# Optimization experiments

Measured on AMD Instinct MI355X. Metric: run time of the kernel, lower is better.

Reference implementation:

```python
import jax, jax.numpy as jnp
import numpy as np

B, T, D, H = 2, 2048, 1024, 16
DK = D // H  # 64, head dim (even, required by RoPE pairing)


def setup_inputs() -> dict:
    key = jax.random.key(0)
    ks = jax.random.split(key, 9)
    sc = 1.0 / np.sqrt(D)
    x = jax.random.normal(ks[0], (B, T, D), jnp.float32)
    wq = jax.random.normal(ks[1], (D, D), jnp.float32) * sc
    bq = jax.random.normal(ks[2], (D,), jnp.float32) * 0.01
    wk = jax.random.normal(ks[3], (D, D), jnp.float32) * sc
    bk = jax.random.normal(ks[4], (D,), jnp.float32) * 0.01
    wv = jax.random.normal(ks[5], (D, D), jnp.float32) * sc
    bv = jax.random.normal(ks[6], (D,), jnp.float32) * 0.01
    wo = jax.random.normal(ks[7], (D, D), jnp.float32) * sc
    bo = jax.random.normal(ks[8], (D,), jnp.float32) * 0.01
    # causal mask, True = masked (matches masked_fill semantics); dim==3 -> broadcast over heads
    attn_mask = jnp.triu(jnp.ones((T, T), dtype=bool), 1)[None]  # [1,T,T]
    return dict(x=x, wq=wq, bq=bq, wk=wk, bk=bk, wv=wv, bv=bv, wo=wo, bo=bo,
                attn_mask=attn_mask)


def _rope(xh, sin, cos):
    # xh: [B,H,T,DK]; sin/cos: [T,DK/2]
    x1 = xh[..., 0::2]
    x2 = xh[..., 1::2]
    return jnp.stack([x1 * cos - x2 * sin, x1 * sin + x2 * cos], axis=-1).reshape(xh.shape)


def reference(x, wq, bq, wk, bk, wv, bv, wo, bo, attn_mask):
    q = (x @ wq.T + bq).reshape(B, T, H, DK).transpose(0, 2, 1, 3)  # [B,H,T,DK]
    k = (x @ wk.T + bk).reshape(B, T, H, DK).transpose(0, 2, 1, 3)
    v = (x @ wv.T + bv).reshape(B, T, H, DK).transpose(0, 2, 1, 3)
    # RoPE (seq_offset = 0)
    theta = 10000.0 ** (jnp.arange(0, DK, 2, dtype=jnp.float32) / DK)  # [DK/2]
    pos = jnp.arange(T, dtype=jnp.float32)[:, None]                    # [T,1]
    ang = pos / theta                                                  # [T,DK/2]
    sin, cos = jnp.sin(ang), jnp.cos(ang)
    q = _rope(q, sin, cos)
    k = _rope(k, sin, cos)
    # fp32 stable attention (inputs already fp32)
    scores = jnp.einsum('bhtd,bhsd->bhts', q, k) / np.sqrt(DK)
    scores = jnp.where(attn_mask[:, None], -1e9, scores)  # mask broadcast over heads
    attn = jax.nn.softmax(scores, axis=-1)
    ctx = jnp.einsum('bhts,bhsd->bhtd', attn, v)
    ctx = ctx.transpose(0, 2, 1, 3).reshape(B, T, D)
    return ctx @ wo.T + bo
```

## Files before the change

kernel.cpp:

```cpp
#include <hip/hip_runtime.h>
#include <stdint.h>
#include <stddef.h>

#define T_ 2048
#define D_ 1024
#define H_ 16

typedef __attribute__((ext_vector_type(8))) short short8;
typedef __attribute__((ext_vector_type(4))) float f32x4;
typedef __attribute__((ext_vector_type(4))) short s16x4;

__device__ __forceinline__ unsigned short f2bf(float f){
  union { float f; unsigned u; } c; c.f = f;
  unsigned u = c.u;
  return (unsigned short)((u + 0x7fffu + ((u >> 16) & 1u)) >> 16);
}

__device__ __forceinline__ unsigned pk_bf16(float lo, float hi){
  unsigned r;
  asm("v_cvt_pk_bf16_f32 %0, %1, %2" : "=v"(r) : "v"(lo), "v"(hi));
  return r;
}

__device__ __forceinline__ float fexp2(float x){
#if __has_builtin(__builtin_amdgcn_exp2f)
  return __builtin_amdgcn_exp2f(x);
#else
  return exp2f(x);
#endif
}

__device__ __forceinline__ f32x4 mfma16(short8 a, short8 b, f32x4 c){
  return __builtin_amdgcn_mfma_f32_16x16x32_bf16(a, b, c, 0, 0, 0);
}

__device__ __forceinline__ void gload16(const void* g, void* l){
  __builtin_amdgcn_global_load_lds(
      (const __attribute__((address_space(1))) unsigned*)g,
      (__attribute__((address_space(3))) unsigned*)l, 16, 0, 0);
}

__global__ __launch_bounds__(256) void k_prep(const float* __restrict__ x,
    const float* __restrict__ wq, const float* __restrict__ wk,
    const float* __restrict__ wv, const float* __restrict__ wo,
    unsigned short* __restrict__ xb, unsigned short* __restrict__ wqkv,
    unsigned short* __restrict__ wob)
{
  const long long NX = 4194304LL, NW = 1048576LL;
  long long base = ((long long)blockIdx.x * 256 + threadIdx.x) * 4;
  const float* s; unsigned short* d;
  if (base < NX){ s = x + base; d = xb + base; }
  else if (base < NX + 3*NW){
    long long j = base - NX;
    if (j < NW) s = wq + j;
    else if (j < 2*NW) s = wk + (j - NW);
    else s = wv + (j - 2*NW);
    d = wqkv + j;
  } else if (base < NX + 4*NW){
    long long j = base - NX - 3*NW;
    s = wo + j; d = wob + j;
  } else return;
  float4 v = *(const float4*)s;
  d[0] = f2bf(v.x); d[1] = f2bf(v.y); d[2] = f2bf(v.z); d[3] = f2bf(v.w);
}

__global__ __launch_bounds__(256) void k_rope(float* __restrict__ tab){
  int i = blockIdx.x * 256 + threadIdx.x;
  if (i >= T_ * 32) return;
  int t = i >> 5, p = i & 31;
  float ang = (float)t * powf(10000.0f, -(float)p * (1.0f / 32.0f));
  tab[i] = sinf(ang);
  tab[T_ * 32 + i] = cosf(ang);
}

__device__ __forceinline__ void gemm_core(const unsigned short* __restrict__ A,
    const unsigned short* __restrict__ Bm, int m0, int n0,
    unsigned short* lA, unsigned short* lB, f32x4 (&acc)[4][4])
{
  const int tid = threadIdx.x, lane = tid & 63, wave = tid >> 6;
  const int wr = wave >> 1, wc = wave & 1;
  for (int mi = 0; mi < 4; ++mi)
    for (int ni = 0; ni < 4; ++ni)
      acc[mi][ni] = (f32x4){0.f, 0.f, 0.f, 0.f};
  for (int k0 = 0; k0 < 1024; k0 += 64){
    __syncthreads();
#pragma unroll
    for (int p = 0; p < 4; ++p){
      int c = p * 256 + tid, r = c >> 3, s = c & 7;
      int gs = (s ^ (r & 7)) << 3;
      gload16(A + (size_t)(m0 + r) * 1024 + k0 + gs, lA + c * 8);
      gload16(Bm + (size_t)(n0 + r) * 1024 + k0 + gs, lB + c * 8);
    }
    __syncthreads();
#pragma unroll
    for (int kk = 0; kk < 2; ++kk){
      int kslot = kk * 4 + (lane >> 4);
      short8 af[4], bf[4];
#pragma unroll
      for (int mi = 0; mi < 4; ++mi){
        int row = wr * 64 + mi * 16 + (lane & 15);
        af[mi] = *(const short8*)(lA + row * 64 + ((kslot ^ (row & 7)) << 3));
      }
#pragma unroll
      for (int ni = 0; ni < 4; ++ni){
        int row = wc * 64 + ni * 16 + (lane & 15);
        bf[ni] = *(const short8*)(lB + row * 64 + ((kslot ^ (row & 7)) << 3));
      }
#pragma unroll
      for (int mi = 0; mi < 4; ++mi)
#pragma unroll
        for (int ni = 0; ni < 4; ++ni)
          acc[mi][ni] = mfma16(af[mi], bf[ni], acc[mi][ni]);
    }
  }
}

__global__ __launch_bounds__(256) void k_qkv(const unsigned short* __restrict__ xb,
    const unsigned short* __restrict__ wqkv,
    const float* __restrict__ bq, const float* __restrict__ bk, const float* __restrict__ bv,
    const float* __restrict__ tab,
    unsigned short* __restrict__ Qw, unsigned short* __restrict__ Kw,
    unsigned short* __restrict__ Vw)
{
  __shared__ alignas(16) unsigned short lA[128 * 64];
  __shared__ alignas(16) unsigned short lB[128 * 64];
  int m0 = blockIdx.y * 128, n0 = blockIdx.x * 128;
  f32x4 acc[4][4];
  gemm_core(xb, wqkv, m0, n0, lA, lB, acc);
  int lane = threadIdx.x & 63, wave = threadIdx.x >> 6;
  int wr = wave >> 1, wc = wave & 1;
  int mat = n0 >> 10;
  const float* bias = (mat == 0) ? bq : (mat == 1 ? bk : bv);
  const float* st = tab; const float* ct = tab + T_ * 32;
  if (mat < 2){
    unsigned short* Out = (mat == 0) ? Qw : Kw;
    float qs = (mat == 0) ? 0.18033688011116f : 1.0f;
    for (int mi = 0; mi < 4; ++mi){
      for (int ni = 0; ni < 4; ++ni){
        int col = n0 + wc * 64 + ni * 16 + (lane & 15);
        int nn = col & 1023, h = nn >> 6, dd = nn & 63;
        float bsv = bias[nn];
        f32x4 v4 = acc[mi][ni];
#pragma unroll
        for (int r = 0; r < 4; ++r){
          int m = m0 + wr * 64 + mi * 16 + ((lane >> 4) << 2) + r;
          int bb = m >> 11, t = m & 2047;
          float v = v4[r] + bsv;
          float u = __shfl_xor(v, 1);
          int p = dd >> 1;
          float sv = st[t * 32 + p], cv = ct[t * 32 + p];
          float res = (dd & 1) ? (u * sv + v * cv) : (v * cv - u * sv);
          Out[((size_t)(bb * H_ + h) * T_ + t) * 64 + dd] = f2bf(res * qs);
        }
      }
    }
  } else {
    for (int mi = 0; mi < 4; ++mi){
      for (int ni = 0; ni < 4; ++ni){
        int col = n0 + wc * 64 + ni * 16 + (lane & 15);
        int nn = col & 1023, h = nn >> 6, dd = nn & 63;
        float bsv = bias[nn];
        int mb = m0 + wr * 64 + mi * 16 + ((lane >> 4) << 2);
        int bb = mb >> 11, t = mb & 2047;
        f32x4 v4 = acc[mi][ni];
        s16x4 o;
#pragma unroll
        for (int r = 0; r < 4; ++r) o[r] = (short)f2bf(v4[r] + bsv);
        *(s16x4*)(Vw + ((size_t)((bb * H_ + h) * 64 + dd)) * T_ + t) = o;
      }
    }
  }
}

__global__ __launch_bounds__(256) void k_attn(const unsigned short* __restrict__ Qw,
    const unsigned short* __restrict__ Kw, const unsigned short* __restrict__ Vt_g,
    unsigned short* __restrict__ ctxb)
{
  __shared__ alignas(16) unsigned short Kl[64 * 64];
  __shared__ alignas(16) unsigned short Vl[64 * 64];
  int qt = (int)gridDim.y - 1 - (int)blockIdx.y;
  int bh = blockIdx.x;
  int tid = threadIdx.x, lane = tid & 63, wave = tid >> 6;
  const unsigned short* Qb = Qw + (size_t)bh * T_ * 64;
  const unsigned short* Kb = Kw + (size_t)bh * T_ * 64;
  const unsigned short* Vb = Vt_g + (size_t)bh * 64 * T_;
  int q0 = qt * 128 + wave * 32;

  short8 qf[2][2];
#pragma unroll
  for (int mi = 0; mi < 2; ++mi){
    const unsigned short* qp = Qb + (size_t)(q0 + mi * 16 + (lane & 15)) * 64 + ((lane >> 4) << 3);
    qf[mi][0] = *(const short8*)qp;
    qf[mi][1] = *(const short8*)(qp + 32);
  }
  float mr[2] = {-1e30f, -1e30f}, lr[2] = {0.f, 0.f};
  f32x4 acc_o[2][4];
#pragma unroll
  for (int mi = 0; mi < 2; ++mi)
#pragma unroll
    for (int df = 0; df < 4; ++df) acc_o[mi][df] = (f32x4){0.f, 0.f, 0.f, 0.f};

  const int src0 = ((lane >> 4) & 1) * 32 + (lane & 15);
  const int src1 = src0 + 16;
  const bool hiHalf = lane >= 32;

  int ntiles = 2 * qt + 2;
  for (int jt = 0; jt < ntiles; ++jt){
    int j0 = jt * 64;
    __syncthreads();
#pragma unroll
    for (int p = 0; p < 2; ++p){
      int c = p * 256 + tid, r = c >> 3, s = c & 7;
      int gs = (s ^ (r & 7)) << 3;
      gload16(Kb + (size_t)(j0 + r) * 64 + gs, Kl + c * 8);
      gload16(Vb + (size_t)r * T_ + j0 + gs, Vl + c * 8);
    }
    __syncthreads();
    if (j0 > q0 + 31) continue;
    bool need_mask = (j0 + 63 > q0);

    f32x4 accs[2][4];
#pragma unroll
    for (int mi = 0; mi < 2; ++mi)
#pragma unroll
      for (int jf = 0; jf < 4; ++jf) accs[mi][jf] = (f32x4){0.f, 0.f, 0.f, 0.f};
#pragma unroll
    for (int kk = 0; kk < 2; ++kk){
      int kslot = kk * 4 + (lane >> 4);
      short8 kf[4];
#pragma unroll
      for (int jf = 0; jf < 4; ++jf){
        int row = jf * 16 + (lane & 15);
        kf[jf] = *(const short8*)(Kl + row * 64 + ((kslot ^ (row & 7)) << 3));
      }
#pragma unroll
      for (int mi = 0; mi < 2; ++mi)
#pragma unroll
        for (int jf = 0; jf < 4; ++jf)
          accs[mi][jf] = mfma16(kf[jf], qf[mi][kk], accs[mi][jf]);
    }

    unsigned w0[2][4], w1[2][4];
#pragma unroll
    for (int mi = 0; mi < 2; ++mi){
      int qa = q0 + mi * 16 + (lane & 15);
      float s[4][4];
      float mx = -1e30f;
#pragma unroll
      for (int jf = 0; jf < 4; ++jf)
#pragma unroll
        for (int r = 0; r < 4; ++r){
          float sv = accs[mi][jf][r];
          if (need_mask){
            int ja = j0 + jf * 16 + ((lane >> 4) << 2) + r;
            if (ja > qa) sv = -1e30f;
          }
          s[jf][r] = sv;
          mx = fmaxf(mx, sv);
        }
      mx = fmaxf(mx, __shfl_xor(mx, 16));
      mx = fmaxf(mx, __shfl_xor(mx, 32));
      float mn = fmaxf(mr[mi], mx);
      float sc = fexp2(mr[mi] - mn);
      mr[mi] = mn;
      float rs = 0.f;
#pragma unroll
      for (int jf = 0; jf < 4; ++jf)
#pragma unroll
        for (int r = 0; r < 4; ++r){
          float pe = fexp2(s[jf][r] - mn);
          s[jf][r] = pe;
          rs += pe;
        }
      rs += __shfl_xor(rs, 16);
      rs += __shfl_xor(rs, 32);
      lr[mi] = lr[mi] * sc + rs;
#pragma unroll
      for (int df = 0; df < 4; ++df){
        f32x4 a = acc_o[mi][df];
        a[0] *= sc; a[1] *= sc; a[2] *= sc; a[3] *= sc;
        acc_o[mi][df] = a;
      }
#pragma unroll
      for (int jf = 0; jf < 4; ++jf){
        w0[mi][jf] = pk_bf16(s[jf][0], s[jf][1]);
        w1[mi][jf] = pk_bf16(s[jf][2], s[jf][3]);
      }
    }

#pragma unroll
    for (int kk = 0; kk < 2; ++kk){
      int jslot = kk * 4 + (lane >> 4);
      short8 vf[4];
#pragma unroll
      for (int df = 0; df < 4; ++df){
        int row = df * 16 + (lane & 15);
        vf[df] = *(const short8*)(Vl + row * 64 + ((jslot ^ (row & 7)) << 3));
      }
#pragma unroll
      for (int mi = 0; mi < 2; ++mi){
        unsigned lo0 = (unsigned)__shfl((int)w0[mi][2*kk],   src0);
        unsigned hi0 = (unsigned)__shfl((int)w0[mi][2*kk+1], src0);
        unsigned lo1 = (unsigned)__shfl((int)w1[mi][2*kk],   src0);
        unsigned hi1 = (unsigned)__shfl((int)w1[mi][2*kk+1], src0);
        unsigned lo2 = (unsigned)__shfl((int)w0[mi][2*kk],   src1);
        unsigned hi2 = (unsigned)__shfl((int)w0[mi][2*kk+1], src1);
        unsigned lo3 = (unsigned)__shfl((int)w1[mi][2*kk],   src1);
        unsigned hi3 = (unsigned)__shfl((int)w1[mi][2*kk+1], src1);
        union { unsigned u[4]; short8 v; } pb;
        pb.u[0] = hiHalf ? hi0 : lo0;
        pb.u[1] = hiHalf ? hi1 : lo1;
        pb.u[2] = hiHalf ? hi2 : lo2;
        pb.u[3] = hiHalf ? hi3 : lo3;
#pragma unroll
        for (int df = 0; df < 4; ++df)
          acc_o[mi][df] = mfma16(vf[df], pb.v, acc_o[mi][df]);
      }
    }
  }

  int bb = bh >> 4, h = bh & 15;
#pragma unroll
  for (int mi = 0; mi < 2; ++mi){
    float inv = 1.0f / lr[mi];
    int t = q0 + mi * 16 + (lane & 15);
#pragma unroll
    for (int df = 0; df < 4; ++df){
      int d0 = df * 16 + ((lane >> 4) << 2);
      f32x4 a = acc_o[mi][df];
      s16x4 o;
#pragma unroll
      for (int r = 0; r < 4; ++r) o[r] = (short)f2bf(a[r] * inv);
      *(s16x4*)(ctxb + ((size_t)(bb * T_ + t)) * 1024 + h * 64 + d0) = o;
    }
  }
}

__global__ __launch_bounds__(256) void k_oproj(const unsigned short* __restrict__ ctxb,
    const unsigned short* __restrict__ wob, const float* __restrict__ bo,
    float* __restrict__ out)
{
  __shared__ alignas(16) unsigned short lA[128 * 64];
  __shared__ alignas(16) unsigned short lB[128 * 64];
  int m0 = blockIdx.y * 128, n0 = blockIdx.x * 128;
  f32x4 acc[4][4];
  gemm_core(ctxb, wob, m0, n0, lA, lB, acc);
  int lane = threadIdx.x & 63, wave = threadIdx.x >> 6;
  int wr = wave >> 1, wc = wave & 1;
  for (int mi = 0; mi < 4; ++mi)
    for (int ni = 0; ni < 4; ++ni){
      int col = n0 + wc * 64 + ni * 16 + (lane & 15);
      float bsv = bo[col];
      f32x4 v4 = acc[mi][ni];
#pragma unroll
      for (int r = 0; r < 4; ++r){
        int m = m0 + wr * 64 + mi * 16 + ((lane >> 4) << 2) + r;
        out[(size_t)m * 1024 + col] = v4[r] + bsv;
      }
    }
}

extern "C" void kernel_launch(void* const* d_in, const int* in_sizes, int n_in,
                              void* d_out, int out_size, void* d_ws, size_t ws_size,
                              hipStream_t stream)
{
  const float* x  = (const float*)d_in[0];
  const float* wq = (const float*)d_in[1];
  const float* bq = (const float*)d_in[2];
  const float* wk = (const float*)d_in[3];
  const float* bk = (const float*)d_in[4];
  const float* wv = (const float*)d_in[5];
  const float* bv = (const float*)d_in[6];
  const float* wo = (const float*)d_in[7];
  const float* bo = (const float*)d_in[8];
  char* w = (char*)d_ws;
  unsigned short* xb   = (unsigned short*)(w);
  unsigned short* wqkv = (unsigned short*)(w + (8 << 20));
  unsigned short* wob  = (unsigned short*)(w + (14 << 20));
  unsigned short* Qw   = (unsigned short*)(w + (16 << 20));
  unsigned short* Kw   = (unsigned short*)(w + (24 << 20));
  unsigned short* Vw   = (unsigned short*)(w + (32 << 20));
  unsigned short* ctxb = (unsigned short*)(w + (40 << 20));
  float* tab           = (float*)(w + (48 << 20));

  k_prep<<<8192, 256, 0, stream>>>(x, wq, wk, wv, wo, xb, wqkv, wob);
  k_rope<<<256, 256, 0, stream>>>(tab);
  k_qkv<<<dim3(24, 32), 256, 0, stream>>>(xb, wqkv, bq, bk, bv, tab, Qw, Kw, Vw);
  k_attn<<<dim3(32, 16), 256, 0, stream>>>(Qw, Kw, Vw, ctxb);
  k_oproj<<<dim3(8, 32), 256, 0, stream>>>(ctxb, wob, bo, (float*)d_out);
}
```

Measured before the change: 148.4 us.

## Double-buffer attention K/V tiles, lazy softmax rescale, fuse rope into prep

The attention kernel now double-buffers K/V tiles in shared memory, issuing the next tile's async load before computing the current one, so only one barrier is needed per iteration. It hoists the V fragment reads, raises wave priority around MFMA blocks, and skips the online-softmax rescale unless the running max grows by more than a threshold. The block index is remapped to a 1D swizzled grid to change how work is spread across compute units. The RoPE table generation is folded into the prep kernel, removing one launch. Shared memory use doubles and the lazy rescale lets exponentials exceed 1 by a bounded factor, a small precision risk.

```diff
diff --git a/kernel.cpp b/kernel.cpp
--- a/kernel.cpp
+++ b/kernel.cpp
@@ -44,8 +44,15 @@
     const float* __restrict__ wq, const float* __restrict__ wk,
     const float* __restrict__ wv, const float* __restrict__ wo,
     unsigned short* __restrict__ xb, unsigned short* __restrict__ wqkv,
-    unsigned short* __restrict__ wob)
-{
+    unsigned short* __restrict__ wob, float* __restrict__ tab)
+{
+  if (blockIdx.x < 256){
+    int i = blockIdx.x * 256 + threadIdx.x;
+    int t = i >> 5, p = i & 31;
+    float ang = (float)t * powf(10000.0f, -(float)p * (1.0f / 32.0f));
+    tab[i] = sinf(ang);
+    tab[T_ * 32 + i] = cosf(ang);
+  }
   const long long NX = 4194304LL, NW = 1048576LL;
   long long base = ((long long)blockIdx.x * 256 + threadIdx.x) * 4;
   const float* s; unsigned short* d;
@@ -62,15 +69,6 @@
   } else return;
   float4 v = *(const float4*)s;
   d[0] = f2bf(v.x); d[1] = f2bf(v.y); d[2] = f2bf(v.z); d[3] = f2bf(v.w);
-}
-
-__global__ __launch_bounds__(256) void k_rope(float* __restrict__ tab){
-  int i = blockIdx.x * 256 + threadIdx.x;
-  if (i >= T_ * 32) return;
-  int t = i >> 5, p = i & 31;
-  float ang = (float)t * powf(10000.0f, -(float)p * (1.0f / 32.0f));
-  tab[i] = sinf(ang);
-  tab[T_ * 32 + i] = cosf(ang);
 }
 
 __device__ __forceinline__ void gemm_core(const unsigned short* __restrict__ A,
@@ -176,10 +174,12 @@
     const unsigned short* __restrict__ Kw, const unsigned short* __restrict__ Vt_g,
     unsigned short* __restrict__ ctxb)
 {
-  __shared__ alignas(16) unsigned short Kl[64 * 64];
-  __shared__ alignas(16) unsigned short Vl[64 * 64];
-  int qt = (int)gridDim.y - 1 - (int)blockIdx.y;
-  int bh = blockIdx.x;
+  __shared__ alignas(16) unsigned short Kl[2][64 * 64];
+  __shared__ alignas(16) unsigned short Vl[2][64 * 64];
+  int bid = blockIdx.x;
+  int swz = (bid & 7) * 64 + (bid >> 3);
+  int bh = swz >> 4;
+  int qt = 15 - (swz & 15);
   int tid = threadIdx.x, lane = tid & 63, wave = tid >> 6;
   const unsigned short* Qb = Qw + (size_t)bh * T_ * 64;
   const unsigned short* Kb = Kw + (size_t)bh * T_ * 64;
@@ -203,120 +203,143 @@
   const int src0 = ((lane >> 4) & 1) * 32 + (lane & 15);
   const int src1 = src0 + 16;
   const bool hiHalf = lane >= 32;
-
   int ntiles = 2 * qt + 2;
-  for (int jt = 0; jt < ntiles; ++jt){
-    int j0 = jt * 64;
-    __syncthreads();
+
+  auto STAGE = [&](int jt){
+    int buf = jt & 1, j0 = jt * 64;
+    unsigned short* Kd = (unsigned short*)Kl[buf];
+    unsigned short* Vd = (unsigned short*)Vl[buf];
 #pragma unroll
     for (int p = 0; p < 2; ++p){
       int c = p * 256 + tid, r = c >> 3, s = c & 7;
       int gs = (s ^ (r & 7)) << 3;
-      gload16(Kb + (size_t)(j0 + r) * 64 + gs, Kl + c * 8);
-      gload16(Vb + (size_t)r * T_ + j0 + gs, Vl + c * 8);
+      gload16(Kb + (size_t)(j0 + r) * 64 + gs, Kd + c * 8);
+      gload16(Vb + (size_t)r * T_ + j0 + gs, Vd + c * 8);
+    }
+  };
+
+  STAGE(0);
+  __syncthreads();
+  for (int jt = 0; jt < ntiles; ++jt){
+    if (jt + 1 < ntiles) STAGE(jt + 1);
+    int j0 = jt * 64;
+    if (j0 <= q0 + 31){
+      const unsigned short* Kc = Kl[jt & 1];
+      const unsigned short* Vc = Vl[jt & 1];
+      bool need_mask = (j0 + 63 > q0);
+
+      f32x4 accs[2][4];
+#pragma unroll
+      for (int mi = 0; mi < 2; ++mi)
+#pragma unroll
+        for (int jf = 0; jf < 4; ++jf) accs[mi][jf] = (f32x4){0.f, 0.f, 0.f, 0.f};
+#pragma unroll
+      for (int kk = 0; kk < 2; ++kk){
+        int kslot = kk * 4 + (lane >> 4);
+        short8 kf[4];
+#pragma unroll
+        for (int jf = 0; jf < 4; ++jf){
+          int row = jf * 16 + (lane & 15);
+          kf[jf] = *(const short8*)(Kc + row * 64 + ((kslot ^ (row & 7)) << 3));
+        }
+        __builtin_amdgcn_s_setprio(1);
+#pragma unroll
+        for (int mi = 0; mi < 2; ++mi)
+#pragma unroll
+          for (int jf = 0; jf < 4; ++jf)
+            accs[mi][jf] = mfma16(kf[jf], qf[mi][kk], accs[mi][jf]);
+        __builtin_amdgcn_s_setprio(0);
+      }
+
+      short8 vf[2][4];
+#pragma unroll
+      for (int kk = 0; kk < 2; ++kk){
+        int jslot = kk * 4 + (lane >> 4);
+#pragma unroll
+        for (int df = 0; df < 4; ++df){
+          int row = df * 16 + (lane & 15);
+          vf[kk][df] = *(const short8*)(Vc + row * 64 + ((jslot ^ (row & 7)) << 3));
+        }
+      }
+
+      unsigned w0[2][4], w1[2][4];
+#pragma unroll
+      for (int mi = 0; mi < 2; ++mi){
+        int qa = q0 + mi * 16 + (lane & 15);
+        float s[4][4];
+        float mx = -1e30f;
+#pragma unroll
+        for (int jf = 0; jf < 4; ++jf)
+#pragma unroll
+          for (int r = 0; r < 4; ++r){
+            float sv = accs[mi][jf][r];
+            if (need_mask){
+              int ja = j0 + jf * 16 + ((lane >> 4) << 2) + r;
+              if (ja > qa) sv = -1e30f;
+            }
+            s[jf][r] = sv;
+            mx = fmaxf(mx, sv);
+          }
+        mx = fmaxf(mx, __shfl_xor(mx, 16));
+        mx = fmaxf(mx, __shfl_xor(mx, 32));
+        float mn = mr[mi];
+        if (!__all(mx <= mn + 8.0f)){
+          mn = fmaxf(mn, mx);
+          float sc = fexp2(mr[mi] - mn);
+          mr[mi] = mn;
+          lr[mi] *= sc;
+#pragma unroll
+          for (int df = 0; df < 4; ++df){
+            f32x4 a = acc_o[mi][df];
+            a[0] *= sc; a[1] *= sc; a[2] *= sc; a[3] *= sc;
+            acc_o[mi][df] = a;
+          }
+        }
+        float rs = 0.f;
+#pragma unroll
+        for (int jf = 0; jf < 4; ++jf)
+#pragma unroll
+          for (int r = 0; r < 4; ++r){
+            float pe = fexp2(s[jf][r] - mn);
+            s[jf][r] = pe;
+            rs += pe;
+          }
+        rs += __shfl_xor(rs, 16);
+        rs += __shfl_xor(rs, 32);
+        lr[mi] += rs;
+#pragma unroll
+        for (int jf = 0; jf < 4; ++jf){
+          w0[mi][jf] = pk_bf16(s[jf][0], s[jf][1]);
+          w1[mi][jf] = pk_bf16(s[jf][2], s[jf][3]);
+        }
+      }
+
+#pragma unroll
+      for (int kk = 0; kk < 2; ++kk){
+#pragma unroll
+        for (int mi = 0; mi < 2; ++mi){
+          unsigned lo0 = (unsigned)__shfl((int)w0[mi][2*kk],   src0);
+          unsigned hi0 = (unsigned)__shfl((int)w0[mi][2*kk+1], src0);
+          unsigned lo1 = (unsigned)__shfl((int)w1[mi][2*kk],   src0);
+          unsigned hi1 = (unsigned)__shfl((int)w1[mi][2*kk+1], src0);
+          unsigned lo2 = (unsigned)__shfl((int)w0[mi][2*kk],   src1);
+          unsigned hi2 = (unsigned)__shfl((int)w0[mi][2*kk+1], src1);
+          unsigned lo3 = (unsigned)__shfl((int)w1[mi][2*kk],   src1);
+          unsigned hi3 = (unsigned)__shfl((int)w1[mi][2*kk+1], src1);
+          union { unsigned u[4]; short8 v; } pb;
+          pb.u[0] = hiHalf ? hi0 : lo0;
+          pb.u[1] = hiHalf ? hi1 : lo1;
+          pb.u[2] = hiHalf ? hi2 : lo2;
+          pb.u[3] = hiHalf ? hi3 : lo3;
+          __builtin_amdgcn_s_setprio(1);
+#pragma unroll
+          for (int df = 0; df < 4; ++df)
+            acc_o[mi][df] = mfma16(vf[kk][df], pb.v, acc_o[mi][df]);
+          __builtin_amdgcn_s_setprio(0);
+        }
+      }
     }
     __syncthreads();
-    if (j0 > q0 + 31) continue;
-    bool need_mask = (j0 + 63 > q0);
-
-    f32x4 accs[2][4];
-#pragma unroll
-    for (int mi = 0; mi < 2; ++mi)
-#pragma unroll
-      for (int jf = 0; jf < 4; ++jf) accs[mi][jf] = (f32x4){0.f, 0.f, 0.f, 0.f};
-#pragma unroll
-    for (int kk = 0; kk < 2; ++kk){
-      int kslot = kk * 4 + (lane >> 4);
-      short8 kf[4];
-#pragma unroll
-      for (int jf = 0; jf < 4; ++jf){
-        int row = jf * 16 + (lane & 15);
-        kf[jf] = *(const short8*)(Kl + row * 64 + ((kslot ^ (row & 7)) << 3));
-      }
-#pragma unroll
-      for (int mi = 0; mi < 2; ++mi)
-#pragma unroll
-        for (int jf = 0; jf < 4; ++jf)
-          accs[mi][jf] = mfma16(kf[jf], qf[mi][kk], accs[mi][jf]);
-    }
-
-    unsigned w0[2][4], w1[2][4];
-#pragma unroll
-    for (int mi = 0; mi < 2; ++mi){
-      int qa = q0 + mi * 16 + (lane & 15);
-      float s[4][4];
-      float mx = -1e30f;
-#pragma unroll
-      for (int jf = 0; jf < 4; ++jf)
-#pragma unroll
-        for (int r = 0; r < 4; ++r){
-          float sv = accs[mi][jf][r];
-          if (need_mask){
-            int ja = j0 + jf * 16 + ((lane >> 4) << 2) + r;
-            if (ja > qa) sv = -1e30f;
-          }
-          s[jf][r] = sv;
-          mx = fmaxf(mx, sv);
-        }
-      mx = fmaxf(mx, __shfl_xor(mx, 16));
-      mx = fmaxf(mx, __shfl_xor(mx, 32));
-      float mn = fmaxf(mr[mi], mx);
-      float sc = fexp2(mr[mi] - mn);
-      mr[mi] = mn;
-      float rs = 0.f;
-#pragma unroll
-      for (int jf = 0; jf < 4; ++jf)
-#pragma unroll
-        for (int r = 0; r < 4; ++r){
-          float pe = fexp2(s[jf][r] - mn);
-          s[jf][r] = pe;
-          rs += pe;
-        }
-      rs += __shfl_xor(rs, 16);
-      rs += __shfl_xor(rs, 32);
-      lr[mi] = lr[mi] * sc + rs;
-#pragma unroll
-      for (int df = 0; df < 4; ++df){
-        f32x4 a = acc_o[mi][df];
-        a[0] *= sc; a[1] *= sc; a[2] *= sc; a[3] *= sc;
-        acc_o[mi][df] = a;
-      }
-#pragma unroll
-      for (int jf = 0; jf < 4; ++jf){
-        w0[mi][jf] = pk_bf16(s[jf][0], s[jf][1]);
-        w1[mi][jf] = pk_bf16(s[jf][2], s[jf][3]);
-      }
-    }
-
-#pragma unroll
-    for (int kk = 0; kk < 2; ++kk){
-      int jslot = kk * 4 + (lane >> 4);
-      short8 vf[4];
-#pragma unroll
-      for (int df = 0; df < 4; ++df){
-        int row = df * 16 + (lane & 15);
-        vf[df] = *(const short8*)(Vl + row * 64 + ((jslot ^ (row & 7)) << 3));
-      }
-#pragma unroll
-      for (int mi = 0; mi < 2; ++mi){
-        unsigned lo0 = (unsigned)__shfl((int)w0[mi][2*kk],   src0);
-        unsigned hi0 = (unsigned)__shfl((int)w0[mi][2*kk+1], src0);
-        unsigned lo1 = (unsigned)__shfl((int)w1[mi][2*kk],   src0);
-        unsigned hi1 = (unsigned)__shfl((int)w1[mi][2*kk+1], src0);
-        unsigned lo2 = (unsigned)__shfl((int)w0[mi][2*kk],   src1);
-        unsigned hi2 = (unsigned)__shfl((int)w0[mi][2*kk+1], src1);
-        unsigned lo3 = (unsigned)__shfl((int)w1[mi][2*kk],   src1);
-        unsigned hi3 = (unsigned)__shfl((int)w1[mi][2*kk+1], src1);
-        union { unsigned u[4]; short8 v; } pb;
-        pb.u[0] = hiHalf ? hi0 : lo0;
-        pb.u[1] = hiHalf ? hi1 : lo1;
-        pb.u[2] = hiHalf ? hi2 : lo2;
-        pb.u[3] = hiHalf ? hi3 : lo3;
-#pragma unroll
-        for (int df = 0; df < 4; ++df)
-          acc_o[mi][df] = mfma16(vf[df], pb.v, acc_o[mi][df]);
-      }
-    }
   }
 
   int bb = bh >> 4, h = bh & 15;
@@ -383,9 +406,8 @@
   unsigned short* ctxb = (unsigned short*)(w + (40 << 20));
   float* tab           = (float*)(w + (48 << 20));
 
-  k_prep<<<8192, 256, 0, stream>>>(x, wq, wk, wv, wo, xb, wqkv, wob);
-  k_rope<<<256, 256, 0, stream>>>(tab);
+  k_prep<<<8192, 256, 0, stream>>>(x, wq, wk, wv, wo, xb, wqkv, wob, tab);
   k_qkv<<<dim3(24, 32), 256, 0, stream>>>(xb, wqkv, bq, bk, bv, tab, Qw, Kw, Vw);
-  k_attn<<<dim3(32, 16), 256, 0, stream>>>(Qw, Kw, Vw, ctxb);
+  k_attn<<<512, 256, 0, stream>>>(Qw, Kw, Vw, ctxb);
   k_oproj<<<dim3(8, 32), 256, 0, stream>>>(ctxb, wob, bo, (float*)d_out);
 }
```

Result: slower. 157.9 us (+6.4%).
